# Performance work log

Measured on AMD Instinct MI355X. Metric: run time of the kernel, lower is better.

Reference implementation:

```python
import jax, jax.numpy as jnp
import numpy as np

N_NODES = 100000
N_EDGES = 1600000
D = 64


def setup_inputs() -> dict:
    key = jax.random.key(0)
    k_row, k_col, k_vals, k_h, k_h0, k_w, k_lam, k_al = jax.random.split(key, 8)
    row = jax.random.randint(k_row, (N_EDGES,), 0, N_NODES, dtype=jnp.int32)
    col = jax.random.randint(k_col, (N_EDGES,), 0, N_NODES, dtype=jnp.int32)
    vals = jax.random.uniform(k_vals, (N_EDGES,), dtype=jnp.float32)
    H = jax.random.normal(k_h, (N_NODES, D), dtype=jnp.float32)
    H0 = jax.random.normal(k_h0, (N_NODES, D), dtype=jnp.float32)
    std = 1.0 / np.sqrt(D)
    weight = jax.random.uniform(k_w, (D, D), minval=-std, maxval=std, dtype=jnp.float32)
    lamda = jax.random.uniform(k_lam, (), dtype=jnp.float32)
    alpha = jax.random.uniform(k_al, (), dtype=jnp.float32)
    l = 4  # 1-based layer index
    return {"row": row, "col": col, "vals": vals, "H": H, "H0": H0,
            "weight": weight, "lamda": lamda, "alpha": alpha, "l": l}


def reference(row, col, vals, H, H0, weight, lamda, alpha, l):
    n = H.shape[0]
    beta = jnp.log(lamda / l + 1.0)
    # SPMM over COO adjacency: out[row] += vals * H[col]
    AH = jax.ops.segment_sum(vals[:, None] * H[col], row, num_segments=n)
    support = (1.0 - alpha) * AH + alpha * H0
    return (1.0 - beta) * support + beta * (support @ weight)
```

## Files before the change

### kernel.cpp

```cpp
#include <hip/hip_runtime.h>
#include <hip/hip_bf16.h>
#include <hip/hip_fp16.h>

#define N_NODES 100000
#define N_EDGES 1600000
#define D 64
#define CHUNK 1024
#define NCHUNK ((N_NODES + CHUNK - 1) / CHUNK)

#define NBIN 200
#define RPB  500
#define MS_TILE 4096
#define MS_CAP  48
#define SCAP 8704


__global__ void __launch_bounds__(256)
bin_hist_kernel(const int* __restrict__ row, int* __restrict__ binCounts) {
    __shared__ int h[NBIN];
    if (threadIdx.x < NBIN) h[threadIdx.x] = 0;
    __syncthreads();
    for (int e = blockIdx.x * blockDim.x + threadIdx.x; e < N_EDGES;
         e += gridDim.x * blockDim.x)
        atomicAdd(&h[row[e] / RPB], 1);
    __syncthreads();
    if (threadIdx.x < NBIN) atomicAdd(&binCounts[threadIdx.x], h[threadIdx.x]);
}

__global__ void __launch_bounds__(256)
bin_scan_kernel(const int* __restrict__ binCounts,
                int* __restrict__ binBase, int* __restrict__ binCursor) {
    __shared__ int s[256];
    const int tid = threadIdx.x;
    const int cnt = (tid < NBIN) ? binCounts[tid] : 0;
    s[tid] = cnt;
    __syncthreads();
    for (int off = 1; off < 256; off <<= 1) {
        int t = (tid >= off) ? s[tid - off] : 0;
        __syncthreads();
        s[tid] += t;
        __syncthreads();
    }
    const int excl = s[tid] - cnt;
    if (tid < NBIN) {
        binBase[tid]   = excl;
        binCursor[tid] = excl;
        if (tid == NBIN - 1) binBase[NBIN] = s[tid];
    }
}

__global__ void __launch_bounds__(256)
multisplit_kernel(const int* __restrict__ row, const int* __restrict__ col,
                  const float* __restrict__ vals,
                  int* __restrict__ binCursor,
                  unsigned* __restrict__ tmp4, unsigned short* __restrict__ tmp2) {
    __shared__ unsigned       spay[NBIN][MS_CAP];
    __shared__ unsigned short srow[NBIN][MS_CAP];
    __shared__ int bcnt[NBIN];
    __shared__ int gb[NBIN];

    const int tid = threadIdx.x;
    if (tid < NBIN) bcnt[tid] = 0;
    __syncthreads();

    const int base = blockIdx.x * MS_TILE;
    const int eEnd = min(base + MS_TILE, N_EDGES);

    #pragma unroll
    for (int j = 0; j < MS_TILE / 256; ++j) {
        const int e = base + j * 256 + tid;
        if (e < eEnd) {
            const int r = row[e];
            const int c = col[e];
            __half hv = __float2half_rn(vals[e]);
            unsigned short hb;
            __builtin_memcpy(&hb, &hv, 2);
            const unsigned pk = ((unsigned)c << 15) | (hb & 0x7FFFu);
            const int bin = r / RPB;
            const unsigned short rl = (unsigned short)(r - bin * RPB);
            const int p = atomicAdd(&bcnt[bin], 1);
            if (p < MS_CAP) {
                spay[bin][p] = pk;
                srow[bin][p] = rl;
            } else {
                const int g = atomicAdd(&binCursor[bin], 1);
                tmp4[g] = pk;
                tmp2[g] = rl;
            }
        }
    }
    __syncthreads();

    if (tid < NBIN) {
        const int c = min(bcnt[tid], MS_CAP);
        gb[tid] = atomicAdd(&binCursor[tid], c);
    }
    __syncthreads();

    for (int i = tid; i < NBIN * MS_CAP; i += 256) {
        const int bin  = i / MS_CAP;
        const int slot = i - bin * MS_CAP;
        if (slot < min(bcnt[bin], MS_CAP)) {
            const int g = gb[bin] + slot;
            tmp4[g] = spay[bin][slot];
            tmp2[g] = srow[bin][slot];
        }
    }
}

__global__ void __launch_bounds__(512)
bin_sort_kernel(const int* __restrict__ binBase,
                const unsigned* __restrict__ tmp4, const unsigned short* __restrict__ tmp2,
                int* __restrict__ row_ptr, unsigned* __restrict__ pack) {
    __shared__ unsigned       pay[SCAP];
    __shared__ unsigned short rl[SCAP];
    __shared__ int rcnt[512];
    __shared__ int rex[512];

    const int tid = threadIdx.x;
    const int b    = blockIdx.x;
    const int base = binBase[b];
    const int nb   = binBase[b + 1] - base;
    const int row0 = b * RPB;

    if (tid < 512) rcnt[tid] = 0;
    __syncthreads();

    for (int i = tid; i < nb; i += 512) {
        const unsigned       p = tmp4[base + i];
        const unsigned short r = tmp2[base + i];
        if (i < SCAP) { pay[i] = p; rl[i] = r; }
        atomicAdd(&rcnt[r], 1);
    }
    __syncthreads();

    const int cnt = rcnt[tid];
    rex[tid] = cnt;
    __syncthreads();
    for (int off = 1; off < 512; off <<= 1) {
        int t = (tid >= off) ? rex[tid - off] : 0;
        __syncthreads();
        rex[tid] += t;
        __syncthreads();
    }
    const int excl = rex[tid] - cnt;
    if (tid < RPB) row_ptr[row0 + tid] = base + excl;
    if (b == NBIN - 1 && tid == 0) row_ptr[N_NODES] = N_EDGES;
    __syncthreads();
    rcnt[tid] = excl;
    __syncthreads();

    for (int i = tid; i < nb; i += 512) {
        unsigned p; unsigned short r;
        if (i < SCAP) { p = pay[i]; r = rl[i]; }
        else          { p = tmp4[base + i]; r = tmp2[base + i]; }
        const int d = atomicAdd(&rcnt[r], 1);
        pack[base + d] = p;
    }
}

__global__ void __launch_bounds__(256)
h2half_kernel(const float* __restrict__ H, unsigned short* __restrict__ Hh) {
    const int tid = blockIdx.x * blockDim.x + threadIdx.x;
    const int total = N_NODES * D / 4;
    if (tid >= total) return;
    const float4 f = reinterpret_cast<const float4*>(H)[tid];
    __half2 h01 = __floats2half2_rn(f.x, f.y);
    __half2 h23 = __floats2half2_rn(f.z, f.w);
    uint2 u;
    __builtin_memcpy(&u.x, &h01, 4);
    __builtin_memcpy(&u.y, &h23, 4);
    reinterpret_cast<uint2*>(Hh)[tid] = u;
}

__device__ inline float h_from_bits(unsigned bits) {
    unsigned short us = (unsigned short)bits;
    __half h;
    __builtin_memcpy(&h, &us, 2);
    return __half2float(h);
}

__global__ void __launch_bounds__(256)
gather_gemm_kernel(const int* __restrict__ row_ptr,
                   const unsigned* __restrict__ pack,
                   const unsigned short* __restrict__ Hh,
                   const float* __restrict__ H0,
                   const float* __restrict__ W,
                   const float* __restrict__ lamda_p, const float* __restrict__ alpha_p,
                   const int* __restrict__ l_p,
                   float* __restrict__ out) {
    __shared__ float supT[D][68];
    __shared__ float Wl[D][D];

    const int tid = threadIdx.x;
    for (int i = tid; i < D * D; i += 256) ((float*)Wl)[i] = W[i];

    const float alpha = alpha_p[0];
    const float beta  = logf(lamda_p[0] / (float)l_p[0] + 1.0f);

    const int wave = tid >> 6;
    const int lane = tid & 63;
    const int R0 = blockIdx.x * 64;
    const int rbase = R0 + wave * 16;

    int rpidx = rbase + ((lane < 17) ? lane : 16);
    if (rpidx > N_NODES) rpidx = N_NODES;
    const int rp_l = row_ptr[rpidx];

    for (int i = 0; i < 16; ++i) {
        const int r = rbase + i;
        if (r >= N_NODES) break;
        const int s = __builtin_amdgcn_readlane(rp_l, i);
        const int t = __builtin_amdgcn_readlane(rp_l, i + 1);

        float a0 = 0.f, a1 = 0.f, a2 = 0.f, a3 = 0.f;
        for (int e = s; e < t; e += 16) {
            int ei = e + (lane & 15);
            if (ei > t - 1) ei = t - 1;
            const unsigned p_l = pack[ei];
            #pragma unroll
            for (int k = 0; k < 16; ++k) {
                const unsigned p = (unsigned)__builtin_amdgcn_readlane((int)p_l, k);
                const unsigned vbits = (e + k < t) ? (p & 0x7FFFu) : 0u;
                const float v = h_from_bits(vbits);
                const unsigned short hb = Hh[(size_t)(p >> 15) * D + lane];
                __half hh; __builtin_memcpy(&hh, &hb, 2);
                const float hf = __half2float(hh);
                if ((k & 3) == 0) a0 = fmaf(v, hf, a0);
                else if ((k & 3) == 1) a1 = fmaf(v, hf, a1);
                else if ((k & 3) == 2) a2 = fmaf(v, hf, a2);
                else a3 = fmaf(v, hf, a3);
            }
        }
        const float acc = (a0 + a1) + (a2 + a3);
        const float sup = (1.0f - alpha) * acc + alpha * H0[(size_t)r * D + lane];
        supT[lane][wave * 16 + i] = sup;
    }
    __syncthreads();

    const int ty = tid >> 4;
    const int tx = tid & 15;
    float acc[4][4] = {{0.f}};

    #pragma unroll 8
    for (int k = 0; k < D; ++k) {
        const float4 A = *reinterpret_cast<const float4*>(&supT[k][4 * ty]);
        const float4 B = *reinterpret_cast<const float4*>(&Wl[k][4 * tx]);
        acc[0][0] = fmaf(A.x, B.x, acc[0][0]); acc[0][1] = fmaf(A.x, B.y, acc[0][1]);
        acc[0][2] = fmaf(A.x, B.z, acc[0][2]); acc[0][3] = fmaf(A.x, B.w, acc[0][3]);
        acc[1][0] = fmaf(A.y, B.x, acc[1][0]); acc[1][1] = fmaf(A.y, B.y, acc[1][1]);
        acc[1][2] = fmaf(A.y, B.z, acc[1][2]); acc[1][3] = fmaf(A.y, B.w, acc[1][3]);
        acc[2][0] = fmaf(A.z, B.x, acc[2][0]); acc[2][1] = fmaf(A.z, B.y, acc[2][1]);
        acc[2][2] = fmaf(A.z, B.z, acc[2][2]); acc[2][3] = fmaf(A.z, B.w, acc[2][3]);
        acc[3][0] = fmaf(A.w, B.x, acc[3][0]); acc[3][1] = fmaf(A.w, B.y, acc[3][1]);
        acc[3][2] = fmaf(A.w, B.z, acc[3][2]); acc[3][3] = fmaf(A.w, B.w, acc[3][3]);
    }

    #pragma unroll
    for (int i = 0; i < 4; ++i) {
        const int r = R0 + 4 * ty + i;
        if (r < N_NODES) {
            float4 o;
            o.x = (1.0f - beta) * supT[4 * tx + 0][4 * ty + i] + beta * acc[i][0];
            o.y = (1.0f - beta) * supT[4 * tx + 1][4 * ty + i] + beta * acc[i][1];
            o.z = (1.0f - beta) * supT[4 * tx + 2][4 * ty + i] + beta * acc[i][2];
            o.w = (1.0f - beta) * supT[4 * tx + 3][4 * ty + i] + beta * acc[i][3];
            *reinterpret_cast<float4*>(&out[(size_t)r * D + 4 * tx]) = o;
        }
    }
}

__global__ void hist_kernel(const int* __restrict__ row, int* __restrict__ counts) {
    int e = blockIdx.x * blockDim.x + threadIdx.x;
    if (e >= N_EDGES) return;
    atomicAdd(&counts[row[e]], 1);
}

__global__ void __launch_bounds__(256)
scan1_kernel(const int* __restrict__ counts, int* __restrict__ row_ptr,
             int* __restrict__ chunkTotals) {
    __shared__ int s[256];
    const int t = threadIdx.x;
    const int base = blockIdx.x * CHUNK + t * 4;
    int c0 = (base + 0 < N_NODES) ? counts[base + 0] : 0;
    int c1 = (base + 1 < N_NODES) ? counts[base + 1] : 0;
    int c2 = (base + 2 < N_NODES) ? counts[base + 2] : 0;
    int c3 = (base + 3 < N_NODES) ? counts[base + 3] : 0;
    const int sum = c0 + c1 + c2 + c3;
    s[t] = sum;
    __syncthreads();
    for (int off = 1; off < 256; off <<= 1) {
        int u = (t >= off) ? s[t - off] : 0;
        __syncthreads();
        s[t] += u;
        __syncthreads();
    }
    const int excl = s[t] - sum;
    if (base + 0 < N_NODES) row_ptr[base + 0] = excl;
    if (base + 1 < N_NODES) row_ptr[base + 1] = excl + c0;
    if (base + 2 < N_NODES) row_ptr[base + 2] = excl + c0 + c1;
    if (base + 3 < N_NODES) row_ptr[base + 3] = excl + c0 + c1 + c2;
    if (t == 255) chunkTotals[blockIdx.x] = s[255];
}

__global__ void __launch_bounds__(256)
scan2_kernel(int* __restrict__ row_ptr, int* __restrict__ cursor,
             const int* __restrict__ chunkTotals) {
    int offset = 0;
    for (int i = 0; i < (int)blockIdx.x; ++i) offset += chunkTotals[i];
    const int idx = blockIdx.x * CHUNK + threadIdx.x * 4;
    #pragma unroll
    for (int j = 0; j < 4; ++j) {
        const int k = idx + j;
        if (k < N_NODES) {
            const int v = row_ptr[k] + offset;
            row_ptr[k] = v;
            cursor[k]  = v;
        }
    }
    if (blockIdx.x == 0 && threadIdx.x == 0) row_ptr[N_NODES] = N_EDGES;
}

__global__ void scatter_pack_kernel(const int* __restrict__ row, const int* __restrict__ col,
                                    const float* __restrict__ vals,
                                    int* __restrict__ cursor,
                                    unsigned* __restrict__ pack) {
    int e = blockIdx.x * blockDim.x + threadIdx.x;
    if (e >= N_EDGES) return;
    const int pos = atomicAdd(&cursor[row[e]], 1);
    __half hv = __float2half_rn(vals[e]);
    unsigned short hb;
    __builtin_memcpy(&hb, &hv, 2);
    pack[pos] = ((unsigned)col[e] << 15) | (hb & 0x7FFFu);
}

__global__ void spmm_atomic_kernel(const int* __restrict__ row,
                                   const int* __restrict__ col,
                                   const float* __restrict__ vals,
                                   const float* __restrict__ H,
                                   float* __restrict__ AH) {
    const long long total = (long long)N_EDGES * 16;
    long long idx = (long long)blockIdx.x * blockDim.x + threadIdx.x;
    if (idx >= total) return;
    const int e   = (int)(idx >> 4);
    const int sub = (int)(idx & 15);
    const int r   = row[e];
    const int c   = col[e];
    const float v = vals[e];
    const float4 h = *reinterpret_cast<const float4*>(&H[(long long)c * D + sub * 4]);
    float* dst = &AH[(long long)r * D + sub * 4];
    atomicAdd(dst + 0, v * h.x);
    atomicAdd(dst + 1, v * h.y);
    atomicAdd(dst + 2, v * h.z);
    atomicAdd(dst + 3, v * h.w);
}

__global__ void __launch_bounds__(256)
gcnii_epilogue_kernel(float* __restrict__ AH_out,
                      const float* __restrict__ H0,
                      const float* __restrict__ W,
                      const float* __restrict__ lamda_p,
                      const float* __restrict__ alpha_p,
                      const int* __restrict__ l_p) {
    __shared__ float Wlds[D * D];
    for (int i = threadIdx.x; i < D * D; i += 256) Wlds[i] = W[i];
    __syncthreads();
    const float alpha = alpha_p[0];
    const float beta  = logf(lamda_p[0] / (float)l_p[0] + 1.0f);
    const int wave = threadIdx.x >> 6;
    const int lane = threadIdx.x & 63;
    const int r = blockIdx.x * 4 + wave;
    if (r >= N_NODES) return;
    const long long base = (long long)r * D;
    const float sup = (1.0f - alpha) * AH_out[base + lane] + alpha * H0[base + lane];
    float acc = 0.0f;
    #pragma unroll
    for (int k = 0; k < D; ++k)
        acc = fmaf(__shfl(sup, k, 64), Wlds[k * D + lane], acc);
    AH_out[base + lane] = (1.0f - beta) * sup + beta * acc;
}

extern "C" void kernel_launch(void* const* d_in, const int* in_sizes, int n_in,
                              void* d_out, int out_size, void* d_ws, size_t ws_size,
                              hipStream_t stream) {
    const int*   row   = (const int*)  d_in[0];
    const int*   col   = (const int*)  d_in[1];
    const float* vals  = (const float*)d_in[2];
    const float* H     = (const float*)d_in[3];
    const float* H0    = (const float*)d_in[4];
    const float* W     = (const float*)d_in[5];
    const float* lamda = (const float*)d_in[6];
    const float* alpha = (const float*)d_in[7];
    const int*   l     = (const int*)  d_in[8];
    float* out = (float*)d_out;

    const size_t neededA2 = (size_t)7300800 * 4;
    const size_t neededA  = (size_t)5000256 * 4;
    const size_t neededC  = 0;

    if (ws_size >= neededA2) {
        int*            binCounts = (int*)d_ws;
        int*            binBase   = binCounts + 256;
        int*            binCursor = binCounts + 512;
        int*            row_ptr   = binCounts + 768;
        unsigned*       pack      = (unsigned*)(binCounts + 100800);
        unsigned short* tmp2      = (unsigned short*)(binCounts + 1700800);
        unsigned*       tmp4      = (unsigned*)(binCounts + 2500800);
        unsigned short* Hh        = (unsigned short*)(binCounts + 4100800);

        h2half_kernel<<<(N_NODES * D / 4 + 255) / 256, 256, 0, stream>>>(H, Hh);
        hipMemsetAsync(binCounts, 0, NBIN * sizeof(int), stream);
        bin_hist_kernel<<<256, 256, 0, stream>>>(row, binCounts);
        bin_scan_kernel<<<1, 256, 0, stream>>>(binCounts, binBase, binCursor);
        multisplit_kernel<<<(N_EDGES + MS_TILE - 1) / MS_TILE, 256, 0, stream>>>(
            row, col, vals, binCursor, tmp4, tmp2);
        bin_sort_kernel<<<NBIN, 512, 0, stream>>>(binBase, tmp4, tmp2, row_ptr, pack);
        gather_gemm_kernel<<<(N_NODES + 63) / 64, 256, 0, stream>>>(
            row_ptr, pack, Hh, H0, W, lamda, alpha, l, out);
    } else if (ws_size >= neededA) {
        int*            counts  = (int*)d_ws;
        int*            row_ptr = counts + 100000;
        int*            totals  = counts + 200064;
        unsigned*       pack    = (unsigned*)(counts + 200192);
        unsigned short* Hh      = (unsigned short*)(counts + 1800256);

        h2half_kernel<<<(N_NODES * D / 4 + 255) / 256, 256, 0, stream>>>(H, Hh);
        hipMemsetAsync(counts, 0, (size_t)N_NODES * sizeof(int), stream);
        hist_kernel<<<(N_EDGES + 255) / 256, 256, 0, stream>>>(row, counts);
        scan1_kernel<<<NCHUNK, 256, 0, stream>>>(counts, row_ptr, totals);
        scan2_kernel<<<NCHUNK, 256, 0, stream>>>(row_ptr, counts, totals);
        scatter_pack_kernel<<<(N_EDGES + 255) / 256, 256, 0, stream>>>(row, col, vals,
                                                                       counts, pack);
        gather_gemm_kernel<<<(N_NODES + 63) / 64, 256, 0, stream>>>(
            row_ptr, pack, Hh, H0, W, lamda, alpha, l, out);
    } else {
        hipMemsetAsync(out, 0, (size_t)out_size * sizeof(float), stream);
        const long long total = (long long)N_EDGES * 16;
        spmm_atomic_kernel<<<(int)((total + 255) / 256), 256, 0, stream>>>(row, col, vals, H, out);
        gcnii_epilogue_kernel<<<(N_NODES + 3) / 4, 256, 0, stream>>>(out, H0, W,
                                                                     lamda, alpha, l);
    }
}
```

Baseline: 143.4 us.

## Fuse H half-conversion with bin histogram, fold bin scan into consumers, add prefetch

```diff
diff --git a/kernel.cpp b/kernel.cpp
--- a/kernel.cpp
+++ b/kernel.cpp
@@ -14,53 +14,61 @@
 #define MS_CAP  48
 #define SCAP 8704
 
-
-__global__ void __launch_bounds__(256)
-bin_hist_kernel(const int* __restrict__ row, int* __restrict__ binCounts) {
+typedef float f32x4 __attribute__((ext_vector_type(4)));
+
+template <typename T>
+__device__ __forceinline__ T ntl(const T* p) { return __builtin_nontemporal_load(p); }
+
+
+__global__ void __launch_bounds__(256)
+h2h_hist_kernel(const float* __restrict__ H, unsigned short* __restrict__ Hh,
+                const int* __restrict__ row, int* __restrict__ binCounts) {
+    const int total4 = N_NODES * D / 4;
+    for (int i = blockIdx.x * blockDim.x + threadIdx.x; i < total4;
+         i += gridDim.x * blockDim.x) {
+        const f32x4 f = ntl(reinterpret_cast<const f32x4*>(H) + i);
+        __half2 h01 = __floats2half2_rn(f.x, f.y);
+        __half2 h23 = __floats2half2_rn(f.z, f.w);
+        uint2 u;
+        __builtin_memcpy(&u.x, &h01, 4);
+        __builtin_memcpy(&u.y, &h23, 4);
+        reinterpret_cast<uint2*>(Hh)[i] = u;
+    }
     __shared__ int h[NBIN];
     if (threadIdx.x < NBIN) h[threadIdx.x] = 0;
     __syncthreads();
     for (int e = blockIdx.x * blockDim.x + threadIdx.x; e < N_EDGES;
          e += gridDim.x * blockDim.x)
-        atomicAdd(&h[row[e] / RPB], 1);
+        atomicAdd(&h[ntl(row + e) / RPB], 1);
     __syncthreads();
     if (threadIdx.x < NBIN) atomicAdd(&binCounts[threadIdx.x], h[threadIdx.x]);
-}
-
-__global__ void __launch_bounds__(256)
-bin_scan_kernel(const int* __restrict__ binCounts,
-                int* __restrict__ binBase, int* __restrict__ binCursor) {
-    __shared__ int s[256];
-    const int tid = threadIdx.x;
-    const int cnt = (tid < NBIN) ? binCounts[tid] : 0;
-    s[tid] = cnt;
-    __syncthreads();
-    for (int off = 1; off < 256; off <<= 1) {
-        int t = (tid >= off) ? s[tid - off] : 0;
-        __syncthreads();
-        s[tid] += t;
-        __syncthreads();
-    }
-    const int excl = s[tid] - cnt;
-    if (tid < NBIN) {
-        binBase[tid]   = excl;
-        binCursor[tid] = excl;
-        if (tid == NBIN - 1) binBase[NBIN] = s[tid];
-    }
 }
 
 __global__ void __launch_bounds__(256)
 multisplit_kernel(const int* __restrict__ row, const int* __restrict__ col,
                   const float* __restrict__ vals,
-                  int* __restrict__ binCursor,
+                  const int* __restrict__ binCounts,
+                  int* __restrict__ relCur,
                   unsigned* __restrict__ tmp4, unsigned short* __restrict__ tmp2) {
     __shared__ unsigned       spay[NBIN][MS_CAP];
     __shared__ unsigned short srow[NBIN][MS_CAP];
     __shared__ int bcnt[NBIN];
     __shared__ int gb[NBIN];
+    __shared__ int sBase[NBIN];
+    __shared__ int sc[256];
 
     const int tid = threadIdx.x;
-    if (tid < NBIN) bcnt[tid] = 0;
+
+    const int c = (tid < NBIN) ? binCounts[tid] : 0;
+    sc[tid] = c;
+    __syncthreads();
+    for (int off = 1; off < 256; off <<= 1) {
+        int t = (tid >= off) ? sc[tid - off] : 0;
+        __syncthreads();
+        sc[tid] += t;
+        __syncthreads();
+    }
+    if (tid < NBIN) { sBase[tid] = sc[tid] - c; bcnt[tid] = 0; }
     __syncthreads();
 
     const int base = blockIdx.x * MS_TILE;
@@ -70,30 +78,30 @@
     for (int j = 0; j < MS_TILE / 256; ++j) {
         const int e = base + j * 256 + tid;
         if (e < eEnd) {
-            const int r = row[e];
-            const int c = col[e];
-            __half hv = __float2half_rn(vals[e]);
+            const int r = ntl(row + e);
+            const int cc = ntl(col + e);
+            __half hv = __float2half_rn(ntl(vals + e));
             unsigned short hb;
             __builtin_memcpy(&hb, &hv, 2);
-            const unsigned pk = ((unsigned)c << 15) | (hb & 0x7FFFu);
+            const unsigned pk = ((unsigned)cc << 15) | (hb & 0x7FFFu);
             const int bin = r / RPB;
-            const unsigned short rl = (unsigned short)(r - bin * RPB);
+            const unsigned short rlcl = (unsigned short)(r - bin * RPB);
             const int p = atomicAdd(&bcnt[bin], 1);
             if (p < MS_CAP) {
                 spay[bin][p] = pk;
-                srow[bin][p] = rl;
+                srow[bin][p] = rlcl;
             } else {
-                const int g = atomicAdd(&binCursor[bin], 1);
-                tmp4[g] = pk;
-                tmp2[g] = rl;
+                const int g = sBase[bin] + atomicAdd(&relCur[bin], 1);
+                __builtin_nontemporal_store(pk, tmp4 + g);
+                __builtin_nontemporal_store(rlcl, tmp2 + g);
             }
         }
     }
     __syncthreads();
 
     if (tid < NBIN) {
-        const int c = min(bcnt[tid], MS_CAP);
-        gb[tid] = atomicAdd(&binCursor[tid], c);
+        const int cc = min(bcnt[tid], MS_CAP);
+        gb[tid] = sBase[tid] + atomicAdd(&relCur[tid], cc);
     }
     __syncthreads();
 
@@ -102,33 +110,45 @@
         const int slot = i - bin * MS_CAP;
         if (slot < min(bcnt[bin], MS_CAP)) {
             const int g = gb[bin] + slot;
-            tmp4[g] = spay[bin][slot];
-            tmp2[g] = srow[bin][slot];
+            __builtin_nontemporal_store(spay[bin][slot], tmp4 + g);
+            __builtin_nontemporal_store(srow[bin][slot], tmp2 + g);
         }
     }
 }
 
 __global__ void __launch_bounds__(512)
-bin_sort_kernel(const int* __restrict__ binBase,
+bin_sort_kernel(const int* __restrict__ binCounts,
                 const unsigned* __restrict__ tmp4, const unsigned short* __restrict__ tmp2,
                 int* __restrict__ row_ptr, unsigned* __restrict__ pack) {
     __shared__ unsigned       pay[SCAP];
     __shared__ unsigned short rl[SCAP];
     __shared__ int rcnt[512];
     __shared__ int rex[512];
+    __shared__ int base_nb[2];
 
     const int tid = threadIdx.x;
-    const int b    = blockIdx.x;
-    const int base = binBase[b];
-    const int nb   = binBase[b + 1] - base;
+    const int b = blockIdx.x;
+
+    if (tid < 256) rex[tid] = (tid < NBIN) ? binCounts[tid] : 0;
+    __syncthreads();
+    for (int off = 1; off < 256; off <<= 1) {
+        int t = (tid < 256 && tid >= off) ? rex[tid - off] : 0;
+        __syncthreads();
+        if (tid < 256) rex[tid] += t;
+        __syncthreads();
+    }
+    if (tid == 0) { base_nb[0] = rex[b] - binCounts[b]; base_nb[1] = binCounts[b]; }
+    __syncthreads();
+    const int base = base_nb[0];
+    const int nb   = base_nb[1];
     const int row0 = b * RPB;
 
-    if (tid < 512) rcnt[tid] = 0;
+    rcnt[tid] = 0;
     __syncthreads();
 
     for (int i = tid; i < nb; i += 512) {
-        const unsigned       p = tmp4[base + i];
-        const unsigned short r = tmp2[base + i];
+        const unsigned       p = ntl(tmp4 + base + i);
+        const unsigned short r = ntl(tmp2 + base + i);
         if (i < SCAP) { pay[i] = p; rl[i] = r; }
         atomicAdd(&rcnt[r], 1);
     }
@@ -153,24 +173,10 @@
     for (int i = tid; i < nb; i += 512) {
         unsigned p; unsigned short r;
         if (i < SCAP) { p = pay[i]; r = rl[i]; }
-        else          { p = tmp4[base + i]; r = tmp2[base + i]; }
+        else          { p = ntl(tmp4 + base + i); r = ntl(tmp2 + base + i); }
         const int d = atomicAdd(&rcnt[r], 1);
-        pack[base + d] = p;
-    }
-}
-
-__global__ void __launch_bounds__(256)
-h2half_kernel(const float* __restrict__ H, unsigned short* __restrict__ Hh) {
-    const int tid = blockIdx.x * blockDim.x + threadIdx.x;
-    const int total = N_NODES * D / 4;
-    if (tid >= total) return;
-    const float4 f = reinterpret_cast<const float4*>(H)[tid];
-    __half2 h01 = __floats2half2_rn(f.x, f.y);
-    __half2 h23 = __floats2half2_rn(f.z, f.w);
-    uint2 u;
-    __builtin_memcpy(&u.x, &h01, 4);
-    __builtin_memcpy(&u.y, &h23, 4);
-    reinterpret_cast<uint2*>(Hh)[tid] = u;
+        __builtin_nontemporal_store(p, pack + base + d);
+    }
 }
 
 __device__ inline float h_from_bits(unsigned bits) {
@@ -213,15 +219,29 @@
         const int s = __builtin_amdgcn_readlane(rp_l, i);
         const int t = __builtin_amdgcn_readlane(rp_l, i + 1);
 
+        const float h0v = ntl(&H0[(size_t)r * D + lane]);
+
         float a0 = 0.f, a1 = 0.f, a2 = 0.f, a3 = 0.f;
-        for (int e = s; e < t; e += 16) {
-            int ei = e + (lane & 15);
+        unsigned p_l = 0;
+        if (s < t) {
+            int ei = s + (lane & 15);
             if (ei > t - 1) ei = t - 1;
-            const unsigned p_l = pack[ei];
+            p_l = ntl(pack + ei);
+        }
+        int e = s;
+        while (e < t) {
+            const int ebase = e;
+            const unsigned p_cur = p_l;
+            e += 16;
+            if (e < t) {
+                int ei = e + (lane & 15);
+                if (ei > t - 1) ei = t - 1;
+                p_l = ntl(pack + ei);
+            }
             #pragma unroll
             for (int k = 0; k < 16; ++k) {
-                const unsigned p = (unsigned)__builtin_amdgcn_readlane((int)p_l, k);
-                const unsigned vbits = (e + k < t) ? (p & 0x7FFFu) : 0u;
+                const unsigned p = (unsigned)__builtin_amdgcn_readlane((int)p_cur, k);
+                const unsigned vbits = (ebase + k < t) ? (p & 0x7FFFu) : 0u;
                 const float v = h_from_bits(vbits);
                 const unsigned short hb = Hh[(size_t)(p >> 15) * D + lane];
                 __half hh; __builtin_memcpy(&hh, &hb, 2);
@@ -233,7 +253,7 @@
             }
         }
         const float acc = (a0 + a1) + (a2 + a3);
-        const float sup = (1.0f - alpha) * acc + alpha * H0[(size_t)r * D + lane];
+        const float sup = (1.0f - alpha) * acc + alpha * h0v;
         supT[lane][wave * 16 + i] = sup;
     }
     __syncthreads();
@@ -260,14 +280,29 @@
     for (int i = 0; i < 4; ++i) {
         const int r = R0 + 4 * ty + i;
         if (r < N_NODES) {
-            float4 o;
+            f32x4 o;
             o.x = (1.0f - beta) * supT[4 * tx + 0][4 * ty + i] + beta * acc[i][0];
             o.y = (1.0f - beta) * supT[4 * tx + 1][4 * ty + i] + beta * acc[i][1];
             o.z = (1.0f - beta) * supT[4 * tx + 2][4 * ty + i] + beta * acc[i][2];
             o.w = (1.0f - beta) * supT[4 * tx + 3][4 * ty + i] + beta * acc[i][3];
-            *reinterpret_cast<float4*>(&out[(size_t)r * D + 4 * tx]) = o;
-        }
-    }
+            __builtin_nontemporal_store(o,
+                reinterpret_cast<f32x4*>(&out[(size_t)r * D + 4 * tx]));
+        }
+    }
+}
+
+__global__ void __launch_bounds__(256)
+h2half_kernel(const float* __restrict__ H, unsigned short* __restrict__ Hh) {
+    const int tid = blockIdx.x * blockDim.x + threadIdx.x;
+    const int total = N_NODES * D / 4;
+    if (tid >= total) return;
+    const float4 f = reinterpret_cast<const float4*>(H)[tid];
+    __half2 h01 = __floats2half2_rn(f.x, f.y);
+    __half2 h23 = __floats2half2_rn(f.z, f.w);
+    uint2 u;
+    __builtin_memcpy(&u.x, &h01, 4);
+    __builtin_memcpy(&u.y, &h23, 4);
+    reinterpret_cast<uint2*>(Hh)[tid] = u;
 }
 
 __global__ void hist_kernel(const int* __restrict__ row, int* __restrict__ counts) {
@@ -394,27 +429,23 @@
     const int*   l     = (const int*)  d_in[8];
     float* out = (float*)d_out;
 
-    const size_t neededA2 = (size_t)7300800 * 4;
+    const size_t neededA2 = (size_t)7300608 * 4;
     const size_t neededA  = (size_t)5000256 * 4;
-    const size_t neededC  = 0;
 
     if (ws_size >= neededA2) {
         int*            binCounts = (int*)d_ws;
-        int*            binBase   = binCounts + 256;
-        int*            binCursor = binCounts + 512;
-        int*            row_ptr   = binCounts + 768;
-        unsigned*       pack      = (unsigned*)(binCounts + 100800);
-        unsigned short* tmp2      = (unsigned short*)(binCounts + 1700800);
-        unsigned*       tmp4      = (unsigned*)(binCounts + 2500800);
-        unsigned short* Hh        = (unsigned short*)(binCounts + 4100800);
-
-        h2half_kernel<<<(N_NODES * D / 4 + 255) / 256, 256, 0, stream>>>(H, Hh);
-        hipMemsetAsync(binCounts, 0, NBIN * sizeof(int), stream);
-        bin_hist_kernel<<<256, 256, 0, stream>>>(row, binCounts);
-        bin_scan_kernel<<<1, 256, 0, stream>>>(binCounts, binBase, binCursor);
+        int*            relCur    = binCounts + 256;
+        int*            row_ptr   = binCounts + 512;
+        unsigned*       pack      = (unsigned*)(binCounts + 100608);
+        unsigned short* tmp2      = (unsigned short*)(binCounts + 1700608);
+        unsigned*       tmp4      = (unsigned*)(binCounts + 2500608);
+        unsigned short* Hh        = (unsigned short*)(binCounts + 4100608);
+
+        hipMemsetAsync(binCounts, 0, 512 * sizeof(int), stream);
+        h2h_hist_kernel<<<512, 256, 0, stream>>>(H, Hh, row, binCounts);
         multisplit_kernel<<<(N_EDGES + MS_TILE - 1) / MS_TILE, 256, 0, stream>>>(
-            row, col, vals, binCursor, tmp4, tmp2);
-        bin_sort_kernel<<<NBIN, 512, 0, stream>>>(binBase, tmp4, tmp2, row_ptr, pack);
+            row, col, vals, binCounts, relCur, tmp4, tmp2);
+        bin_sort_kernel<<<NBIN, 512, 0, stream>>>(binCounts, tmp4, tmp2, row_ptr, pack);
         gather_gemm_kernel<<<(N_NODES + 63) / 64, 256, 0, stream>>>(
             row_ptr, pack, Hh, H0, W, lamda, alpha, l, out);
     } else if (ws_size >= neededA) {
```

Result: slower. 197.0 us (+37.3%).
